# Performance work log

Measured on AMD Instinct MI355X. Metric: run time of the kernel, lower is better.

Reference implementation:

```python
import jax, jax.numpy as jnp
import numpy as np

K = 9
EPS = 1e-8
TAU2D = 2.0
BASE = jnp.array([[-1, -1], [0, -1], [1, -1], [-1, 0], [0, 0], [1, 0], [-1, 1], [0, 1], [1, 1]], dtype=jnp.float32)


def setup_inputs() -> dict:
    key = jax.random.key(0)
    ks = jax.random.split(key, 8)
    B, C, H, W, N = 4, 64, 256, 256, 16384
    hid, out_dim = 64, 1 + 1 + 2 * K + K
    feat_map = jax.random.normal(ks[0], (B, C, H, W), dtype=jnp.float32)
    coords_2d = jax.random.uniform(ks[1], (B, N, 2), dtype=jnp.float32) * 2.0 - 1.0  # normalized [-1,1]
    cell_2d = jax.random.uniform(ks[2], (B, N, 2), dtype=jnp.float32) * 0.02
    W1 = jax.random.normal(ks[3], (C + 4, hid), dtype=jnp.float32) * 0.05
    b1 = jnp.zeros((hid,), dtype=jnp.float32)
    Wr = jax.random.normal(ks[4], (hid, hid), dtype=jnp.float32) * 0.05
    br = jnp.zeros((hid,), dtype=jnp.float32)
    W2 = jax.random.normal(ks[5], (hid, out_dim), dtype=jnp.float32) * 0.05
    b2 = jnp.zeros((out_dim,), dtype=jnp.float32)
    return {"feat_map": feat_map, "coords_2d": coords_2d, "cell_2d": cell_2d,
            "W1": W1, "b1": b1, "Wr": Wr, "br": br, "W2": W2, "b2": b2}


def _grid_sample_1(feat, grid):
    # feat: (C,H,W), grid: (P,2) normalized coords, bilinear, border pad, align_corners=True
    C, H, W = feat.shape
    ix = jnp.clip((grid[:, 0] + 1.0) * 0.5 * (W - 1), 0.0, W - 1)
    iy = jnp.clip((grid[:, 1] + 1.0) * 0.5 * (H - 1), 0.0, H - 1)
    x0 = jnp.floor(ix)
    y0 = jnp.floor(iy)
    wx = ix - x0
    wy = iy - y0
    x0i = x0.astype(jnp.int32)
    y0i = y0.astype(jnp.int32)
    x1i = jnp.minimum(x0i + 1, W - 1)
    y1i = jnp.minimum(y0i + 1, H - 1)
    f00 = feat[:, y0i, x0i]  # (C,P)
    f01 = feat[:, y0i, x1i]
    f10 = feat[:, y1i, x0i]
    f11 = feat[:, y1i, x1i]
    return (f00 * (1 - wx) * (1 - wy) + f01 * wx * (1 - wy)
            + f10 * (1 - wx) * wy + f11 * wx * wy)  # (C,P)


_grid_sample = jax.vmap(_grid_sample_1)  # (B,C,H,W),(B,P,2)->(B,C,P)


def _leaky(x):
    return jnp.where(x >= 0, x, 0.2 * x)


def _forward(feat_map, coords_2d, cell_2d, W1, b1, Wr, br, W2, b2):
    B, C, H, W = feat_map.shape
    N = coords_2d.shape[1]
    # anchor features
    f_anchor = _grid_sample(feat_map, coords_2d).transpose(0, 2, 1)  # (B,N,C)
    router_in = jnp.concatenate([f_anchor, coords_2d, cell_2d], axis=-1)  # (B,N,C+4)
    h = _leaky(router_in @ W1 + b1)
    h = _leaky(h + (h @ Wr + br))  # residual block
    out = h @ W2 + b2  # (B,N,29)
    r_raw = out[..., 0:1]
    sigma_raw = out[..., 1:2]
    res_raw = out[..., 2:2 + 2 * K]
    gate_raw = out[..., 2 + 2 * K:2 + 3 * K]
    r = jnp.clip(jax.nn.softplus(r_raw) + 0.1, 0.1, 4.0)  # (B,N,1)
    sigma = jnp.clip(jax.nn.softplus(sigma_raw) + 0.5, 0.5, 6.0)  # (B,N,1)
    res = jnp.tanh(res_raw).reshape(B, N, K, 2) * 0.5
    offsets_pix = r[:, :, :, None] * BASE[None, None] + res  # (B,N,K,2)
    scale = jnp.array([2.0 / max(W - 1, 1), 2.0 / max(H - 1, 1)], dtype=jnp.float32)
    offsets_norm = offsets_pix * scale
    deform = coords_2d[:, :, None, :] + offsets_norm  # (B,N,K,2)
    f = _grid_sample(feat_map, deform.reshape(B, N * K, 2))  # (B,C,N*K)
    f = f.reshape(B, C, N, K).transpose(0, 2, 3, 1)  # (B,N,K,C)
    d2 = offsets_pix[..., 0] ** 2 + offsets_pix[..., 1] ** 2  # (B,N,K)
    sig_eff = sigma * TAU2D  # (B,N,1)
    w_geo = jnp.exp(-0.5 * d2 / (sig_eff ** 2 + EPS))
    gate = jax.nn.sigmoid(gate_raw)
    w = w_geo * gate
    w = w / (jnp.sum(w, axis=-1, keepdims=True) + EPS)
    out_feat = jnp.einsum('bnkc,bnk->bnc', f, w)
    return out_feat


def reference(feat_map, coords_2d, cell_2d, W1, b1, Wr, br, W2, b2):
    return _forward(feat_map, coords_2d, cell_2d, W1, b1, Wr, br, W2, b2)
```

## Files before the change

kernel.cpp:

```cpp
#include <hip/hip_runtime.h>

#define K_TAPS 9
#define CC 64
#define HH 256
#define WW 256
#define BB 4
#define NN 16384
#define NPTS (BB * NN)
#define SCLX (2.0f / 255.0f)
#define SCLY (2.0f / 255.0f)
#define AS 68

__device__ __forceinline__ float softplus_f(float x) {
    return fmaxf(x, 0.0f) + log1pf(expf(-fabsf(x)));
}
__device__ __forceinline__ float leaky_f(float x) { return x >= 0.0f ? x : 0.2f * x; }
__device__ __forceinline__ float clampf(float x, float lo, float hi) {
    return fminf(fmaxf(x, lo), hi);
}
__device__ __forceinline__ float bf2f(unsigned short u) {
    union { unsigned int i; float f; } v;
    v.i = (unsigned int)u << 16;
    return v.f;
}
__device__ __forceinline__ unsigned short f2bf(float f) {
    union { float f; unsigned int i; } v;
    v.f = f;
    unsigned int r = (v.i + 0x7FFFu + ((v.i >> 16) & 1u)) >> 16;
    return (unsigned short)r;
}

__global__ void __launch_bounds__(256) transpose_kernel(const float* __restrict__ feat,
                                                        unsigned int* __restrict__ featB) {
    __shared__ float tile[64][65];
    int b = blockIdx.y;
    int p0 = blockIdx.x * 64;
    int tp = threadIdx.x & 63;
    int tq = threadIdx.x >> 6;
    const float* fb = feat + (size_t)b * CC * HH * WW;
#pragma unroll
    for (int i = 0; i < 16; ++i) {
        int c = tq * 16 + i;
        tile[c][tp] = fb[(size_t)c * (HH * WW) + p0 + tp];
    }
    __syncthreads();
    unsigned int* ob = featB + ((size_t)b * (HH * WW) + p0) * 32;
    int c2 = threadIdx.x & 31;
    int psub = threadIdx.x >> 5;
#pragma unroll
    for (int i = 0; i < 8; ++i) {
        int p = i * 8 + psub;
        unsigned int lo = f2bf(tile[2 * c2][p]);
        unsigned int hi = f2bf(tile[2 * c2 + 1][p]);
        ob[(size_t)p * 32 + c2] = lo | (hi << 16);
    }
}

__device__ __forceinline__ float4 bilin4_bf(const unsigned short* __restrict__ base, float gx,
                                            float gy, int c4) {
    float ix = clampf((gx + 1.0f) * 0.5f * 255.0f, 0.0f, 255.0f);
    float iy = clampf((gy + 1.0f) * 0.5f * 255.0f, 0.0f, 255.0f);
    float x0f = floorf(ix), y0f = floorf(iy);
    float wx = ix - x0f, wy = iy - y0f;
    int x0 = (int)x0f, y0 = (int)y0f;
    int x1 = min(x0 + 1, 255), y1 = min(y0 + 1, 255);
    const ushort4 u00 = *(const ushort4*)(base + (size_t)(((y0 << 8) + x0) * 64) + c4 * 4);
    const ushort4 u01 = *(const ushort4*)(base + (size_t)(((y0 << 8) + x1) * 64) + c4 * 4);
    const ushort4 u10 = *(const ushort4*)(base + (size_t)(((y1 << 8) + x0) * 64) + c4 * 4);
    const ushort4 u11 = *(const ushort4*)(base + (size_t)(((y1 << 8) + x1) * 64) + c4 * 4);
    float w00 = (1.0f - wx) * (1.0f - wy), w01 = wx * (1.0f - wy);
    float w10 = (1.0f - wx) * wy, w11 = wx * wy;
    float4 v;
    v.x = bf2f(u00.x) * w00 + bf2f(u01.x) * w01 + bf2f(u10.x) * w10 + bf2f(u11.x) * w11;
    v.y = bf2f(u00.y) * w00 + bf2f(u01.y) * w01 + bf2f(u10.y) * w10 + bf2f(u11.y) * w11;
    v.z = bf2f(u00.z) * w00 + bf2f(u01.z) * w01 + bf2f(u10.z) * w10 + bf2f(u11.z) * w11;
    v.w = bf2f(u00.w) * w00 + bf2f(u01.w) * w01 + bf2f(u10.w) * w10 + bf2f(u11.w) * w11;
    return v;
}

__global__ void __launch_bounds__(256, 4) fused_kernel(const unsigned short* __restrict__ featB,
                                                       const float* __restrict__ coords,
                                                       const float* __restrict__ cell,
                                                       const float* __restrict__ W1,
                                                       const float* __restrict__ b1,
                                                       const float* __restrict__ Wr,
                                                       const float* __restrict__ br,
                                                       const float* __restrict__ W2,
                                                       const float* __restrict__ b2,
                                                       float4* __restrict__ out4) {
    __shared__ __align__(16) float act[68 * AS];
    __shared__ __align__(16) float wbuf[68 * 64];
    float4* wbuf4 = (float4*)wbuf;

    const int t = threadIdx.x;
    const int q = t & 15;
    const int pgrp = t >> 4;
    const int blk0 = blockIdx.x * 64;

    {
        const int pt = t & 63;
        const int wvi = t >> 6;
        const int pg = blk0 + pt;
        const int bb2 = pg >> 14;
        const float gx = coords[2 * pg], gy = coords[2 * pg + 1];

        const float4* w1g = (const float4*)W1;
        float4 w1r0 = w1g[t];
        float4 w1r1 = w1g[t + 256];
        float4 w1r2 = w1g[t + 512];
        float4 w1r3 = w1g[t + 768];
        float4 w1x;
        if (t < 64) w1x = w1g[1024 + t];

        float ix = clampf((gx + 1.0f) * 0.5f * 255.0f, 0.0f, 255.0f);
        float iy = clampf((gy + 1.0f) * 0.5f * 255.0f, 0.0f, 255.0f);
        float x0f = floorf(ix), y0f = floorf(iy);
        float wx = ix - x0f, wy = iy - y0f;
        int x0 = (int)x0f, y0 = (int)y0f;
        int x1 = min(x0 + 1, 255), y1 = min(y0 + 1, 255);
        const unsigned short* base = featB + (size_t)bb2 * (HH * WW) * 64;
        size_t i00 = (size_t)(((y0 << 8) + x0) * 64), i01 = (size_t)(((y0 << 8) + x1) * 64);
        size_t i10 = (size_t)(((y1 << 8) + x0) * 64), i11 = (size_t)(((y1 << 8) + x1) * 64);
        ushort4 u00[4], u01[4], u10[4], u11[4];
#pragma unroll
        for (int g = 0; g < 4; ++g) {
            int qq = 4 * g + wvi;
            u00[g] = *(const ushort4*)(base + i00 + qq * 4);
            u01[g] = *(const ushort4*)(base + i01 + qq * 4);
            u10[g] = *(const ushort4*)(base + i10 + qq * 4);
            u11[g] = *(const ushort4*)(base + i11 + qq * 4);
        }

        wbuf4[t] = w1r0;
        wbuf4[t + 256] = w1r1;
        wbuf4[t + 512] = w1r2;
        wbuf4[t + 768] = w1r3;
        if (t < 64) wbuf4[1024 + t] = w1x;

        float w00 = (1.0f - wx) * (1.0f - wy), w01 = wx * (1.0f - wy);
        float w10 = (1.0f - wx) * wy, w11 = wx * wy;
#pragma unroll
        for (int g = 0; g < 4; ++g) {
            int qq = 4 * g + wvi;
            act[(4 * qq + 0) * AS + pt] = bf2f(u00[g].x) * w00 + bf2f(u01[g].x) * w01 +
                                          bf2f(u10[g].x) * w10 + bf2f(u11[g].x) * w11;
            act[(4 * qq + 1) * AS + pt] = bf2f(u00[g].y) * w00 + bf2f(u01[g].y) * w01 +
                                          bf2f(u10[g].y) * w10 + bf2f(u11[g].y) * w11;
            act[(4 * qq + 2) * AS + pt] = bf2f(u00[g].z) * w00 + bf2f(u01[g].z) * w01 +
                                          bf2f(u10[g].z) * w10 + bf2f(u11[g].z) * w11;
            act[(4 * qq + 3) * AS + pt] = bf2f(u00[g].w) * w00 + bf2f(u01[g].w) * w01 +
                                          bf2f(u10[g].w) * w10 + bf2f(u11[g].w) * w11;
        }
        if (wvi == 0) {
            act[64 * AS + pt] = gx;
            act[65 * AS + pt] = gy;
            act[66 * AS + pt] = cell[2 * pg];
            act[67 * AS + pt] = cell[2 * pg + 1];
        }
    }
    __syncthreads();

    const float4* wrg = (const float4*)Wr;
    float4 wrp0 = wrg[t];
    float4 wrp1 = wrg[t + 256];
    float4 wrp2 = wrg[t + 512];
    float4 wrp3 = wrg[t + 768];

    float hres[4][4];
    {
        float acc[4][4];
        float4 b4 = ((const float4*)b1)[q];
        float bj[4] = {b4.x, b4.y, b4.z, b4.w};
#pragma unroll
        for (int j = 0; j < 4; ++j)
#pragma unroll
            for (int p = 0; p < 4; ++p) acc[j][p] = bj[j];
#pragma unroll 4
        for (int i = 0; i < 68; ++i) {
            float4 av = *(const float4*)&act[i * AS + 4 * pgrp];
            float4 wv4 = *(const float4*)&wbuf[i * 64 + 4 * q];
            float a[4] = {av.x, av.y, av.z, av.w};
            float wj[4] = {wv4.x, wv4.y, wv4.z, wv4.w};
#pragma unroll
            for (int j = 0; j < 4; ++j)
#pragma unroll
                for (int p = 0; p < 4; ++p) acc[j][p] = fmaf(a[p], wj[j], acc[j][p]);
        }
#pragma unroll
        for (int j = 0; j < 4; ++j)
#pragma unroll
            for (int p = 0; p < 4; ++p) hres[j][p] = leaky_f(acc[j][p]);
    }
    __syncthreads();

#pragma unroll
    for (int j = 0; j < 4; ++j)
        *(float4*)&act[(4 * q + j) * AS + 4 * pgrp] =
            make_float4(hres[j][0], hres[j][1], hres[j][2], hres[j][3]);
    wbuf4[t] = wrp0;
    wbuf4[t + 256] = wrp1;
    wbuf4[t + 512] = wrp2;
    wbuf4[t + 768] = wrp3;
    __syncthreads();

    const float4* w2g = (const float4*)W2;
    float4 w2p0, w2p1;
    if (t < 232) {
        w2p0 = w2g[t];
        w2p1 = w2g[t + 232];
    }

    float h2[4][4];
    {
        float4 b4 = ((const float4*)br)[q];
        float bj[4] = {b4.x, b4.y, b4.z, b4.w};
#pragma unroll
        for (int j = 0; j < 4; ++j)
#pragma unroll
            for (int p = 0; p < 4; ++p) h2[j][p] = bj[j];
#pragma unroll 4
        for (int i = 0; i < 64; ++i) {
            float4 av = *(const float4*)&act[i * AS + 4 * pgrp];
            float4 wv4 = *(const float4*)&wbuf[i * 64 + 4 * q];
            float a[4] = {av.x, av.y, av.z, av.w};
            float wj[4] = {wv4.x, wv4.y, wv4.z, wv4.w};
#pragma unroll
            for (int j = 0; j < 4; ++j)
#pragma unroll
                for (int p = 0; p < 4; ++p) h2[j][p] = fmaf(a[p], wj[j], h2[j][p]);
        }
#pragma unroll
        for (int j = 0; j < 4; ++j)
#pragma unroll
            for (int p = 0; p < 4; ++p) h2[j][p] = leaky_f(hres[j][p] + h2[j][p]);
    }
    __syncthreads();

#pragma unroll
    for (int j = 0; j < 4; ++j)
        *(float4*)&act[(4 * q + j) * AS + 4 * pgrp] =
            make_float4(h2[j][0], h2[j][1], h2[j][2], h2[j][3]);
    if (t < 232) {
        wbuf4[t] = w2p0;
        wbuf4[t + 232] = w2p1;
    }
    __syncthreads();

    float* sot = wbuf + 2048;
    float* prm = wbuf;

    {
        const int j0 = 2 * q, j1 = 2 * q + 1;
        const int jj0 = min(j0, 28), jj1 = min(j1, 28);
        float o0[4], o1[4];
        float bb0 = b2[jj0], bb1 = b2[jj1];
#pragma unroll
        for (int p = 0; p < 4; ++p) {
            o0[p] = bb0;
            o1[p] = bb1;
        }
#pragma unroll 4
        for (int i = 0; i < 64; ++i) {
            float4 av = *(const float4*)&act[i * AS + 4 * pgrp];
            float a[4] = {av.x, av.y, av.z, av.w};
            float w0 = wbuf[i * 29 + jj0], w1 = wbuf[i * 29 + jj1];
#pragma unroll
            for (int p = 0; p < 4; ++p) {
                o0[p] = fmaf(a[p], w0, o0[p]);
                o1[p] = fmaf(a[p], w1, o1[p]);
            }
        }
#pragma unroll
        for (int p = 0; p < 4; ++p) {
            int pt = 4 * pgrp + p;
            if (j0 < 29) sot[pt * 30 + j0] = o0[p];
            if (j1 < 29) sot[pt * 30 + j1] = o1[p];
        }
    }
    __syncthreads();

    {
        const int pt = t >> 2, sub = t & 3;
        const int pg = blk0 + pt;
        const float* so = sot + pt * 30;
        float gx = coords[2 * pg], gy = coords[2 * pg + 1];
        float r = clampf(softplus_f(so[0]) + 0.1f, 0.1f, 4.0f);
        float sg = clampf(softplus_f(so[1]) + 0.5f, 0.5f, 6.0f);
        float se = sg * 2.0f;
        float inv2 = -0.5f / (se * se + 1e-8f);
        float sx[3], sy[3], wv[3];
        float s = 0.0f;
#pragma unroll
        for (int ii = 0; ii < 3; ++ii) {
            int kr = 4 * ii + sub;
            int k = kr < 9 ? kr : 0;
            float bx = (float)(k % 3 - 1);
            float by = (float)(k / 3 - 1);
            float ox = fmaf(r, bx, tanhf(so[2 + 2 * k]) * 0.5f);
            float oy = fmaf(r, by, tanhf(so[3 + 2 * k]) * 0.5f);
            float d2 = ox * ox + oy * oy;
            float wgeo = expf(d2 * inv2);
            float gate = 1.0f / (1.0f + expf(-so[20 + k]));
            float w = (kr < 9) ? wgeo * gate : 0.0f;
            wv[ii] = w;
            s += w;
            sx[ii] = fmaf(ox, SCLX, gx);
            sy[ii] = fmaf(oy, SCLY, gy);
        }
        s += __shfl_xor(s, 1, 64);
        s += __shfl_xor(s, 2, 64);
        float inv = 1.0f / (s + 1e-8f);
        float* pp = prm + pt * 28;
#pragma unroll
        for (int ii = 0; ii < 3; ++ii) {
            int kr = 4 * ii + sub;
            if (kr < 9) {
                pp[3 * kr + 0] = sx[ii];
                pp[3 * kr + 1] = sy[ii];
                pp[3 * kr + 2] = wv[ii] * inv;
            }
        }
    }
    __syncthreads();

#pragma unroll
    for (int g2 = 0; g2 < 4; ++g2) {
        int task = g2 * 256 + t;
        int c4 = task & 15;
        int pt = task >> 4;
        int pg = blk0 + pt;
        int bb2 = pg >> 14;
        const unsigned short* base = featB + (size_t)bb2 * (HH * WW) * 64;
        const float* pp = prm + pt * 28;
        float4 acc = make_float4(0.0f, 0.0f, 0.0f, 0.0f);
#pragma unroll 3
        for (int k = 0; k < K_TAPS; ++k) {
            float sx = pp[3 * k + 0];
            float sy = pp[3 * k + 1];
            float wk = pp[3 * k + 2];
            float4 v = bilin4_bf(base, sx, sy, c4);
            acc.x = fmaf(v.x, wk, acc.x);
            acc.y = fmaf(v.y, wk, acc.y);
            acc.z = fmaf(v.z, wk, acc.z);
            acc.w = fmaf(v.w, wk, acc.w);
        }
        out4[(size_t)pg * 16 + c4] = acc;
    }
}

__device__ __forceinline__ float bilin_chw(const float* __restrict__ feat, int b, int lane,
                                           float gx, float gy) {
    float ix = clampf((gx + 1.0f) * 0.5f * 255.0f, 0.0f, 255.0f);
    float iy = clampf((gy + 1.0f) * 0.5f * 255.0f, 0.0f, 255.0f);
    float x0f = floorf(ix), y0f = floorf(iy);
    float wx = ix - x0f, wy = iy - y0f;
    int x0 = (int)x0f, y0 = (int)y0f;
    int x1 = min(x0 + 1, 255), y1 = min(y0 + 1, 255);
    const float* base = feat + ((size_t)b * CC + lane) * (HH * WW);
    float f00 = base[(y0 << 8) + x0];
    float f01 = base[(y0 << 8) + x1];
    float f10 = base[(y1 << 8) + x0];
    float f11 = base[(y1 << 8) + x1];
    float omx = 1.0f - wx, omy = 1.0f - wy;
    return (f00 * omx + f01 * wx) * omy + (f10 * omx + f11 * wx) * wy;
}

__global__ void __launch_bounds__(256) fallback_kernel(const float* __restrict__ feat,
                                                       const float* __restrict__ coords,
                                                       const float* __restrict__ cell,
                                                       const float* __restrict__ W1,
                                                       const float* __restrict__ b1,
                                                       const float* __restrict__ Wr,
                                                       const float* __restrict__ br,
                                                       const float* __restrict__ W2,
                                                       const float* __restrict__ b2,
                                                       float* __restrict__ out) {
    int lane = threadIdx.x & 63;
    int wave = threadIdx.x >> 6;
    int pidx = blockIdx.x * 4 + wave;
    if (pidx >= NPTS) return;
    int b = pidx >> 14;
    float gx = coords[(size_t)pidx * 2 + 0];
    float gy = coords[(size_t)pidx * 2 + 1];
    float cx = cell[(size_t)pidx * 2 + 0];
    float cy = cell[(size_t)pidx * 2 + 1];
    float fa = bilin_chw(feat, b, lane, gx, gy);
    float h = b1[lane];
#pragma unroll
    for (int i = 0; i < 64; ++i) {
        float a = __shfl(fa, i, 64);
        h = fmaf(a, W1[i * 64 + lane], h);
    }
    h = fmaf(gx, W1[64 * 64 + lane], h);
    h = fmaf(gy, W1[65 * 64 + lane], h);
    h = fmaf(cx, W1[66 * 64 + lane], h);
    h = fmaf(cy, W1[67 * 64 + lane], h);
    h = leaky_f(h);
    float h2 = br[lane];
#pragma unroll
    for (int i = 0; i < 64; ++i) {
        float a = __shfl(h, i, 64);
        h2 = fmaf(a, Wr[i * 64 + lane], h2);
    }
    h2 = leaky_f(h + h2);
    int j = lane < 29 ? lane : 0;
    float o = b2[j];
#pragma unroll
    for (int i = 0; i < 64; ++i) {
        float a = __shfl(h2, i, 64);
        o = fmaf(a, W2[i * 29 + j], o);
    }
    int kk = lane < K_TAPS ? lane : 0;
    float r_raw = __shfl(o, 0, 64);
    float s_raw = __shfl(o, 1, 64);
    float rx_raw = __shfl(o, 2 + 2 * kk, 64);
    float ry_raw = __shfl(o, 3 + 2 * kk, 64);
    float g_raw = __shfl(o, 20 + kk, 64);
    float r = clampf(softplus_f(r_raw) + 0.1f, 0.1f, 4.0f);
    float sg = clampf(softplus_f(s_raw) + 0.5f, 0.5f, 6.0f);
    float bx = (float)(kk % 3 - 1);
    float by = (float)(kk / 3 - 1);
    float offx = fmaf(r, bx, tanhf(rx_raw) * 0.5f);
    float offy = fmaf(r, by, tanhf(ry_raw) * 0.5f);
    float d2 = offx * offx + offy * offy;
    float se = sg * 2.0f;
    float wgeo = expf(-0.5f * d2 / (se * se + 1e-8f));
    float gate = 1.0f / (1.0f + expf(-g_raw));
    float w = wgeo * gate;
    float wv = (lane < K_TAPS) ? w : 0.0f;
#pragma unroll
    for (int m = 32; m >= 1; m >>= 1) wv += __shfl_xor(wv, m, 64);
    float wn = w / (wv + 1e-8f);
    float acc = 0.0f;
#pragma unroll
    for (int k = 0; k < K_TAPS; ++k) {
        float ox = __shfl(offx, k, 64) * SCLX;
        float oy = __shfl(offy, k, 64) * SCLY;
        float wk2 = __shfl(wn, k, 64);
        float fv = bilin_chw(feat, b, lane, gx + ox, gy + oy);
        acc = fmaf(fv, wk2, acc);
    }
    out[(size_t)pidx * CC + lane] = acc;
}

extern "C" void kernel_launch(void* const* d_in, const int* in_sizes, int n_in,
                              void* d_out, int out_size, void* d_ws, size_t ws_size,
                              hipStream_t stream) {
    const float* feat = (const float*)d_in[0];
    const float* coords = (const float*)d_in[1];
    const float* cell = (const float*)d_in[2];
    const float* W1 = (const float*)d_in[3];
    const float* b1 = (const float*)d_in[4];
    const float* Wr = (const float*)d_in[5];
    const float* br = (const float*)d_in[6];
    const float* W2 = (const float*)d_in[7];
    const float* b2 = (const float*)d_in[8];
    float* out = (float*)d_out;

    const size_t needT = (size_t)BB * HH * WW * CC * sizeof(unsigned short);

    if (ws_size >= needT) {
        unsigned short* featB = (unsigned short*)d_ws;
        dim3 tg((HH * WW) / 64, BB);
        transpose_kernel<<<tg, 256, 0, stream>>>(feat, (unsigned int*)featB);
        fused_kernel<<<NPTS / 64, 256, 0, stream>>>(featB, coords, cell, W1, b1, Wr, br, W2,
                                                    b2, (float4*)out);
    } else {
        fallback_kernel<<<NPTS / 4, 256, 0, stream>>>(feat, coords, cell, W1, b1, Wr, br, W2,
                                                      b2, out);
    }
}
```

Baseline: 72.96 us.

## Sort query points into spatial buckets before fused gather kernel

Adds a counting sort (zero, count, scan, scatter kernels) that groups query points by batch and 16x16 pixel tile, and the fused kernel processes points in that sorted order. The goal is better cache locality for the bilinear gathers from the channel-last bf16 feature map. The cost is four extra small kernel launches, atomics, and scattered output writes. The order within a bucket is nondeterministic, but each output is still written to its own point index.

```diff
diff --git a/kernel.cpp b/kernel.cpp
--- a/kernel.cpp
+++ b/kernel.cpp
@@ -10,6 +10,7 @@
 #define SCLX (2.0f / 255.0f)
 #define SCLY (2.0f / 255.0f)
 #define AS 68
+#define NBKT 1024
 
 __device__ __forceinline__ float softplus_f(float x) {
     return fmaxf(x, 0.0f) + log1pf(expf(-fabsf(x)));
@@ -28,6 +29,58 @@
     v.f = f;
     unsigned int r = (v.i + 0x7FFFu + ((v.i >> 16) & 1u)) >> 16;
     return (unsigned short)r;
+}
+
+__global__ void __launch_bounds__(256) zero_kernel(int* __restrict__ counts) {
+    counts[blockIdx.x * 256 + threadIdx.x] = 0;
+}
+
+__global__ void __launch_bounds__(256) count_kernel(const float* __restrict__ coords,
+                                                    int* __restrict__ bkt,
+                                                    int* __restrict__ counts) {
+    int p = blockIdx.x * 256 + threadIdx.x;
+    float gx = coords[2 * p], gy = coords[2 * p + 1];
+    float ix = clampf((gx + 1.0f) * 0.5f * 255.0f, 0.0f, 255.0f);
+    float iy = clampf((gy + 1.0f) * 0.5f * 255.0f, 0.0f, 255.0f);
+    int tx = (int)ix >> 4;
+    int ty = (int)iy >> 4;
+    int b = p >> 14;
+    int bk = (b << 8) | (ty << 4) | tx;
+    bkt[p] = bk;
+    atomicAdd(&counts[bk], 1);
+}
+
+__global__ void __launch_bounds__(256) scan_kernel(const int* __restrict__ counts,
+                                                   int* __restrict__ offsets) {
+    __shared__ int ls[256];
+    int t = threadIdx.x;
+    int base = t * 4;
+    int v0 = counts[base], v1 = counts[base + 1], v2 = counts[base + 2], v3 = counts[base + 3];
+    int s = v0 + v1 + v2 + v3;
+    ls[t] = s;
+    __syncthreads();
+    for (int off = 1; off < 256; off <<= 1) {
+        int x = (t >= off) ? ls[t - off] : 0;
+        __syncthreads();
+        ls[t] += x;
+        __syncthreads();
+    }
+    int run = ls[t] - s;
+    offsets[base] = run;
+    run += v0;
+    offsets[base + 1] = run;
+    run += v1;
+    offsets[base + 2] = run;
+    run += v2;
+    offsets[base + 3] = run;
+}
+
+__global__ void __launch_bounds__(256) scatter_kernel(const int* __restrict__ bkt,
+                                                      int* __restrict__ offsets,
+                                                      int* __restrict__ order) {
+    int p = blockIdx.x * 256 + threadIdx.x;
+    int pos = atomicAdd(&offsets[bkt[p]], 1);
+    order[pos] = p;
 }
 
 __global__ void __launch_bounds__(256) transpose_kernel(const float* __restrict__ feat,
@@ -79,6 +132,7 @@
 }
 
 __global__ void __launch_bounds__(256, 4) fused_kernel(const unsigned short* __restrict__ featB,
+                                                       const int* __restrict__ order,
                                                        const float* __restrict__ coords,
                                                        const float* __restrict__ cell,
                                                        const float* __restrict__ W1,
@@ -90,6 +144,7 @@
                                                        float4* __restrict__ out4) {
     __shared__ __align__(16) float act[68 * AS];
     __shared__ __align__(16) float wbuf[68 * 64];
+    __shared__ int ordL[64];
     float4* wbuf4 = (float4*)wbuf;
 
     const int t = threadIdx.x;
@@ -97,10 +152,13 @@
     const int pgrp = t >> 4;
     const int blk0 = blockIdx.x * 64;
 
+    if (t < 64) ordL[t] = order[blk0 + t];
+    __syncthreads();
+
     {
         const int pt = t & 63;
         const int wvi = t >> 6;
-        const int pg = blk0 + pt;
+        const int pg = ordL[pt];
         const int bb2 = pg >> 14;
         const float gx = coords[2 * pg], gy = coords[2 * pg + 1];
 
@@ -281,7 +339,7 @@
 
     {
         const int pt = t >> 2, sub = t & 3;
-        const int pg = blk0 + pt;
+        const int pg = ordL[pt];
         const float* so = sot + pt * 30;
         float gx = coords[2 * pg], gy = coords[2 * pg + 1];
         float r = clampf(softplus_f(so[0]) + 0.1f, 0.1f, 4.0f);
@@ -328,7 +386,7 @@
         int task = g2 * 256 + t;
         int c4 = task & 15;
         int pt = task >> 4;
-        int pg = blk0 + pt;
+        int pg = ordL[pt];
         int bb2 = pg >> 14;
         const unsigned short* base = featB + (size_t)bb2 * (HH * WW) * 64;
         const float* pp = prm + pt * 28;
@@ -458,13 +516,28 @@
     float* out = (float*)d_out;
 
     const size_t needT = (size_t)BB * HH * WW * CC * sizeof(unsigned short);
-
-    if (ws_size >= needT) {
+    const size_t offBkt = needT;
+    const size_t offOrd = offBkt + (size_t)NPTS * 4;
+    const size_t offCnt = offOrd + (size_t)NPTS * 4;
+    const size_t offOfs = offCnt + (size_t)NBKT * 4;
+    const size_t needAll = offOfs + (size_t)NBKT * 4;
+
+    if (ws_size >= needAll) {
         unsigned short* featB = (unsigned short*)d_ws;
+        int* bkt = (int*)((char*)d_ws + offBkt);
+        int* order = (int*)((char*)d_ws + offOrd);
+        int* counts = (int*)((char*)d_ws + offCnt);
+        int* offsets = (int*)((char*)d_ws + offOfs);
+
+        zero_kernel<<<NBKT / 256, 256, 0, stream>>>(counts);
+        count_kernel<<<NPTS / 256, 256, 0, stream>>>(coords, bkt, counts);
+        scan_kernel<<<1, 256, 0, stream>>>(counts, offsets);
+        scatter_kernel<<<NPTS / 256, 256, 0, stream>>>(bkt, offsets, order);
+
         dim3 tg((HH * WW) / 64, BB);
         transpose_kernel<<<tg, 256, 0, stream>>>(feat, (unsigned int*)featB);
-        fused_kernel<<<NPTS / 64, 256, 0, stream>>>(featB, coords, cell, W1, b1, Wr, br, W2,
-                                                    b2, (float4*)out);
+        fused_kernel<<<NPTS / 64, 256, 0, stream>>>(featB, order, coords, cell, W1, b1, Wr,
+                                                    br, W2, b2, (float4*)out);
     } else {
         fallback_kernel<<<NPTS / 4, 256, 0, stream>>>(feat, coords, cell, W1, b1, Wr, br, W2,
                                                       b2, out);
```

New measurement: 97.92 us. 34.2% more time.
